# Optimization experiments

Hardware: AMD Instinct MI355X
Metric: run time of the kernel (lower is better)

The kernel has to match this reference:

```python
import jax, jax.numpy as jnp
import numpy as np

# Vehicle / drivetrain constants (match init_kwargs and hard-coded source constants)
LF, LR = 1.5, 1.4
CM1, CM2 = 550.0, 650.0
MASS, IZ = 1265.0, 2000.0
DT = 0.01
C_DRIVE = 3.45 * 0.919 / (0.34 * 1265.0)  # gear-ratio constant from source
GRAV = 9.8


def _mlp(a, w1, b1, w2, b2):
    # 1 -> 12 -> 1 MLP applied per-row. a: [B]; w1,b1,w2: [12]; b2: scalar
    h = jax.nn.relu(a[:, None] * w1[None, :] + b1[None, :])  # [B, 12]
    return h @ w2 + b2  # [B]


def setup_inputs() -> dict:
    key = jax.random.key(0)
    ks = jax.random.split(key, 7)
    B = 4_194_304
    x = jax.random.normal(ks[0], (B, 8), dtype=jnp.float32)
    # First-layer init as in source: weight filled with 1.0, bias = arange(-0.6, 0.6, 0.1)
    b1 = (-0.6 + 0.1 * jnp.arange(12)).astype(jnp.float32)
    bound = float(1.0 / np.sqrt(12.0))  # torch default init bound for Linear(12, 1)
    return {
        "x": x,
        "fy_w1": jnp.ones((12,), jnp.float32),
        "fy_b1": b1,
        "fy_w2": jax.random.uniform(ks[1], (12,), jnp.float32, -bound, bound),
        "fy_b2": jax.random.uniform(ks[2], (), jnp.float32, -bound, bound),
        "ry_w1": jnp.ones((12,), jnp.float32),
        "ry_b1": b1,
        "ry_w2": jax.random.uniform(ks[3], (12,), jnp.float32, -bound, bound),
        "ry_b2": jax.random.uniform(ks[4], (), jnp.float32, -bound, bound),
        "rx_w": jax.random.uniform(ks[5], (), jnp.float32, -1.0, 1.0),
        "rx_b": jax.random.uniform(ks[6], (), jnp.float32, -1.0, 1.0),
    }


def reference(x, fy_w1, fy_b1, fy_w2, fy_b2, ry_w1, ry_b1, ry_w2, ry_b2, rx_w, rx_b):
    pwm = x[:, 0]
    theta = x[:, 2]
    pitch = x[:, 7]
    out = jnp.zeros_like(x[:, 3:6])  # [B, 3] accumulated (dvx, dvy, dw)

    def fy(a):
        return _mlp(a, fy_w1, fy_b1, fy_w2, fy_b2)

    def ry(a):
        return _mlp(a, ry_w1, ry_b1, ry_w2, ry_b2)

    st, ct = jnp.sin(theta), jnp.cos(theta)
    sp = jnp.sin(pitch)
    a_pred = jnp.where(pwm > 0.0, CM1, CM2) * pwm * C_DRIVE

    for _ in range(2):  # fixed 2-step integration loop, as in source
        vx = x[:, 3] + out[:, 0]
        vy = x[:, 4] + out[:, 1]
        w = x[:, 5] + out[:, 2]
        alpha_f = theta - jnp.arctan2(w * LF + vy, vx)
        alpha_r = jnp.arctan2(w * LR - vy, vx)
        # Fy(a)*(a>0) - Fy(-a)*(a<=0): exactly one branch survives per element
        Ffy = jnp.where(alpha_f > 0.0, fy(alpha_f), -fy(-alpha_f))
        Fry = jnp.where(alpha_r > 0.0, ry(alpha_r), -ry(-alpha_r))
        Frx = a_pred + rx_w * vx * vx + rx_b  # Rx(vx^2) + drivetrain accel
        vx_dot = Frx - Ffy * st + vy * w - GRAV * sp
        vy_dot = Fry + Ffy * ct - vx * w
        w_dot = MASS * (Ffy * LF * ct - Fry * LR) / IZ
        out = out + DT * jnp.stack([vx_dot, vy_dot, w_dot], axis=1)
    return out
```

## Files before the change

kernel.cpp:

```cpp
#include <hip/hip_runtime.h>
#include <math.h>

#define DEV_INLINE __device__ __forceinline__

__device__ const float kLF      = 1.5f;
__device__ const float kLR      = 1.4f;
__device__ const float kCM1     = 550.0f;
__device__ const float kCM2     = 650.0f;
__device__ const float kDT      = 0.01f;
__device__ const float kGRAV    = 9.8f;
__device__ const float kCDRIVE  = (float)(3.45 * 0.919 / (0.34 * 1265.0));
__device__ const float kMASS    = 1265.0f;
__device__ const float kIZ_INV  = (float)(1.0 / 2000.0);

DEV_INLINE float mlp12(float a, const float* __restrict__ w1,
                       const float* __restrict__ b1,
                       const float* __restrict__ w2, float b2) {
    float acc = b2;
#pragma unroll
    for (int j = 0; j < 12; ++j) {
        float h = fmaxf(fmaf(a, w1[j], b1[j]), 0.0f);
        acc = fmaf(h, w2[j], acc);
    }
    return acc;
}

__global__ __launch_bounds__(256) void dyn_kernel(
    const float4* __restrict__ x4,
    const float* __restrict__ fy_w1, const float* __restrict__ fy_b1,
    const float* __restrict__ fy_w2, const float* __restrict__ fy_b2,
    const float* __restrict__ ry_w1, const float* __restrict__ ry_b1,
    const float* __restrict__ ry_w2, const float* __restrict__ ry_b2,
    const float* __restrict__ rx_w, const float* __restrict__ rx_b,
    float4* __restrict__ out4, int nrows) {
    float fw1[12], fb1[12], fw2[12];
    float rw1[12], rb1[12], rw2[12];
#pragma unroll
    for (int j = 0; j < 12; ++j) {
        fw1[j] = fy_w1[j]; fb1[j] = fy_b1[j]; fw2[j] = fy_w2[j];
        rw1[j] = ry_w1[j]; rb1[j] = ry_b1[j]; rw2[j] = ry_w2[j];
    }
    const float fb2 = fy_b2[0];
    const float rb2 = ry_b2[0];
    const float rxw = rx_w[0];
    const float rxb = rx_b[0];

    const int t = blockIdx.x * blockDim.x + threadIdx.x;
    const long long base = (long long)t * 4;
    if (base >= nrows) return;

    float4 lo[4], hi[4];
#pragma unroll
    for (int r = 0; r < 4; ++r) {
        lo[r] = x4[(base + r) * 2 + 0];
        hi[r] = x4[(base + r) * 2 + 1];
    }

    float res[12];

#pragma unroll
    for (int r = 0; r < 4; ++r) {
        const float pwm   = lo[r].x;
        const float theta = lo[r].z;
        const float x3    = lo[r].w;
        const float x4v   = hi[r].x;
        const float x5    = hi[r].y;
        const float pitch = hi[r].w;

        const float st = __sinf(theta);
        const float ct = __cosf(theta);
        const float sp = __sinf(pitch);
        const float a_pred = (pwm > 0.0f ? kCM1 : kCM2) * pwm * kCDRIVE;

        float o0 = 0.0f, o1 = 0.0f, o2 = 0.0f;
#pragma unroll
        for (int it = 0; it < 2; ++it) {
            const float vx = x3 + o0;
            const float vy = x4v + o1;
            const float w  = x5 + o2;

            const float af = theta - atan2f(fmaf(w, kLF, vy), vx);
            const float ar = atan2f(fmaf(w, kLR, -vy), vx);

            const float sf  = af > 0.0f ? 1.0f : -1.0f;
            const float Ffy = sf * mlp12(sf * af, fw1, fb1, fw2, fb2);
            const float sr  = ar > 0.0f ? 1.0f : -1.0f;
            const float Fry = sr * mlp12(sr * ar, rw1, rb1, rw2, rb2);

            const float Frx = a_pred + rxw * vx * vx + rxb;

            const float vx_dot = Frx - Ffy * st + vy * w - kGRAV * sp;
            const float vy_dot = Fry + Ffy * ct - vx * w;
            const float w_dot  = kMASS * (Ffy * kLF * ct - Fry * kLR) * kIZ_INV;

            o0 = fmaf(kDT, vx_dot, o0);
            o1 = fmaf(kDT, vy_dot, o1);
            o2 = fmaf(kDT, w_dot,  o2);
        }
        res[r * 3 + 0] = o0;
        res[r * 3 + 1] = o1;
        res[r * 3 + 2] = o2;
    }

#pragma unroll
    for (int k = 0; k < 3; ++k) {
        out4[(long long)t * 3 + k] =
            make_float4(res[k * 4 + 0], res[k * 4 + 1], res[k * 4 + 2], res[k * 4 + 3]);
    }
}

extern "C" void kernel_launch(void* const* d_in, const int* in_sizes, int n_in,
                              void* d_out, int out_size, void* d_ws, size_t ws_size,
                              hipStream_t stream) {
    const float4* x4   = (const float4*)d_in[0];
    const float* fy_w1 = (const float*)d_in[1];
    const float* fy_b1 = (const float*)d_in[2];
    const float* fy_w2 = (const float*)d_in[3];
    const float* fy_b2 = (const float*)d_in[4];
    const float* ry_w1 = (const float*)d_in[5];
    const float* ry_b1 = (const float*)d_in[6];
    const float* ry_w2 = (const float*)d_in[7];
    const float* ry_b2 = (const float*)d_in[8];
    const float* rx_w  = (const float*)d_in[9];
    const float* rx_b  = (const float*)d_in[10];

    const int nrows = in_sizes[0] / 8;
    const int threads = 256;
    const int rows_per_block = threads * 4;
    const int blocks = (nrows + rows_per_block - 1) / rows_per_block;

    dyn_kernel<<<blocks, threads, 0, stream>>>(
        x4, fy_w1, fy_b1, fy_w2, fy_b2, ry_w1, ry_b1, ry_w2, ry_b2, rx_w, rx_b,
        (float4*)d_out, nrows);
}
```

Before: 248.8 us.

## Use polynomial atan2, one row per thread, and LDS-staged coalesced stores

Replaces libm atan2f with a minimax polynomial built on a hardware reciprocal, and cuts the work per thread from four rows to one. Output is staged through shared memory so each block writes contiguous coalesced floats. Constants are folded (mass*arm/Iz) and moved into registers. The polynomial atan2 trades some accuracy for fewer instructions, the one-row mapping launches four times as many blocks, and the shared-memory staging adds a barrier per block.

```diff
diff --git a/kernel.cpp b/kernel.cpp
--- a/kernel.cpp
+++ b/kernel.cpp
@@ -3,15 +3,25 @@
 
 #define DEV_INLINE __device__ __forceinline__
 
-__device__ const float kLF      = 1.5f;
-__device__ const float kLR      = 1.4f;
-__device__ const float kCM1     = 550.0f;
-__device__ const float kCM2     = 650.0f;
-__device__ const float kDT      = 0.01f;
-__device__ const float kGRAV    = 9.8f;
-__device__ const float kCDRIVE  = (float)(3.45 * 0.919 / (0.34 * 1265.0));
-__device__ const float kMASS    = 1265.0f;
-__device__ const float kIZ_INV  = (float)(1.0 / 2000.0);
+DEV_INLINE float fast_atan2f(float y, float x) {
+    const float kPI  = 3.14159265358979323846f;
+    const float kPI2 = 1.57079632679489661923f;
+    float ax = fabsf(x), ay = fabsf(y);
+    float mx = fmaxf(ax, ay);
+    float mn = fminf(ax, ay);
+    float a  = mn * __builtin_amdgcn_rcpf(mx);
+    float s  = a * a;
+    float p  = -0.01172120f;
+    p = fmaf(p, s,  0.05265332f);
+    p = fmaf(p, s, -0.11643287f);
+    p = fmaf(p, s,  0.19354346f);
+    p = fmaf(p, s, -0.33262347f);
+    p = fmaf(p, s,  0.99997726f);
+    float r = a * p;
+    r = (ay > ax)   ? (kPI2 - r) : r;
+    r = (x < 0.0f)  ? (kPI  - r) : r;
+    return copysignf(r, y);
+}
 
 DEV_INLINE float mlp12(float a, const float* __restrict__ w1,
                        const float* __restrict__ b1,
@@ -32,7 +42,19 @@
     const float* __restrict__ ry_w1, const float* __restrict__ ry_b1,
     const float* __restrict__ ry_w2, const float* __restrict__ ry_b2,
     const float* __restrict__ rx_w, const float* __restrict__ rx_b,
-    float4* __restrict__ out4, int nrows) {
+    float* __restrict__ out, int nrows) {
+    const float kLF     = 1.5f;
+    const float kLR     = 1.4f;
+    const float kCM1    = 550.0f;
+    const float kCM2    = 650.0f;
+    const float kDT     = 0.01f;
+    const float kGRAV   = 9.8f;
+    const float kCDRIVE = (float)(3.45 * 0.919 / (0.34 * 1265.0));
+    const float kWF     = (float)(1265.0 * 1.5 / 2000.0);
+    const float kWR     = (float)(1265.0 * 1.4 / 2000.0);
+
+    __shared__ float sout[768];
+
     float fw1[12], fb1[12], fw2[12];
     float rw1[12], rb1[12], rw2[12];
 #pragma unroll
@@ -45,67 +67,63 @@
     const float rxw = rx_w[0];
     const float rxb = rx_b[0];
 
-    const int t = blockIdx.x * blockDim.x + threadIdx.x;
-    const long long base = (long long)t * 4;
-    if (base >= nrows) return;
+    const int tid = threadIdx.x;
+    const long long t = (long long)blockIdx.x * 256 + tid;
 
-    float4 lo[4], hi[4];
-#pragma unroll
-    for (int r = 0; r < 4; ++r) {
-        lo[r] = x4[(base + r) * 2 + 0];
-        hi[r] = x4[(base + r) * 2 + 1];
-    }
+    float o0 = 0.0f, o1 = 0.0f, o2 = 0.0f;
+    if (t < nrows) {
+        const float4 lo = x4[2 * t];
+        const float4 hi = x4[2 * t + 1];
 
-    float res[12];
-
-#pragma unroll
-    for (int r = 0; r < 4; ++r) {
-        const float pwm   = lo[r].x;
-        const float theta = lo[r].z;
-        const float x3    = lo[r].w;
-        const float x4v   = hi[r].x;
-        const float x5    = hi[r].y;
-        const float pitch = hi[r].w;
+        const float pwm   = lo.x;
+        const float theta = lo.z;
+        const float x3    = lo.w;
+        const float x4v   = hi.x;
+        const float x5    = hi.y;
+        const float pitch = hi.w;
 
         const float st = __sinf(theta);
         const float ct = __cosf(theta);
         const float sp = __sinf(pitch);
         const float a_pred = (pwm > 0.0f ? kCM1 : kCM2) * pwm * kCDRIVE;
 
-        float o0 = 0.0f, o1 = 0.0f, o2 = 0.0f;
 #pragma unroll
         for (int it = 0; it < 2; ++it) {
             const float vx = x3 + o0;
             const float vy = x4v + o1;
             const float w  = x5 + o2;
 
-            const float af = theta - atan2f(fmaf(w, kLF, vy), vx);
-            const float ar = atan2f(fmaf(w, kLR, -vy), vx);
+            const float af = theta - fast_atan2f(fmaf(w, kLF, vy), vx);
+            const float ar = fast_atan2f(fmaf(w, kLR, -vy), vx);
 
             const float sf  = af > 0.0f ? 1.0f : -1.0f;
             const float Ffy = sf * mlp12(sf * af, fw1, fb1, fw2, fb2);
             const float sr  = ar > 0.0f ? 1.0f : -1.0f;
             const float Fry = sr * mlp12(sr * ar, rw1, rb1, rw2, rb2);
 
-            const float Frx = a_pred + rxw * vx * vx + rxb;
+            const float Frx = fmaf(rxw * vx, vx, a_pred + rxb);
 
             const float vx_dot = Frx - Ffy * st + vy * w - kGRAV * sp;
             const float vy_dot = Fry + Ffy * ct - vx * w;
-            const float w_dot  = kMASS * (Ffy * kLF * ct - Fry * kLR) * kIZ_INV;
+            const float w_dot  = kWF * Ffy * ct - kWR * Fry;
 
             o0 = fmaf(kDT, vx_dot, o0);
             o1 = fmaf(kDT, vy_dot, o1);
             o2 = fmaf(kDT, w_dot,  o2);
         }
-        res[r * 3 + 0] = o0;
-        res[r * 3 + 1] = o1;
-        res[r * 3 + 2] = o2;
     }
 
+    sout[tid * 3 + 0] = o0;
+    sout[tid * 3 + 1] = o1;
+    sout[tid * 3 + 2] = o2;
+    __syncthreads();
+
+    const long long gbase = (long long)blockIdx.x * 768;
+    const long long gmax  = (long long)nrows * 3;
 #pragma unroll
-    for (int k = 0; k < 3; ++k) {
-        out4[(long long)t * 3 + k] =
-            make_float4(res[k * 4 + 0], res[k * 4 + 1], res[k * 4 + 2], res[k * 4 + 3]);
+    for (int j = 0; j < 3; ++j) {
+        const long long gi = gbase + j * 256 + tid;
+        if (gi < gmax) out[gi] = sout[j * 256 + tid];
     }
 }
 
@@ -126,10 +144,9 @@
 
     const int nrows = in_sizes[0] / 8;
     const int threads = 256;
-    const int rows_per_block = threads * 4;
-    const int blocks = (nrows + rows_per_block - 1) / rows_per_block;
+    const int blocks = (nrows + threads - 1) / threads;
 
     dyn_kernel<<<blocks, threads, 0, stream>>>(
         x4, fy_w1, fy_b1, fy_w2, fy_b2, ry_w1, ry_b1, ry_w2, ry_b2, rx_w, rx_b,
-        (float4*)d_out, nrows);
+        (float*)d_out, nrows);
 }
```

New measurement: 218.5 us. -12.2%, faster.
